# Optimization experiments

Hardware: AMD Instinct MI355X
Metric: run time of the kernel (lower is better)

The kernel has to match this reference:

```python
import jax, jax.numpy as jnp
import numpy as np

ROPE_BASE = 10000.0
NEG_INF = -1e30


def _rope(x, positions):
    """x: [B, heads, D]; positions: [B] int. Matches PrecomputedRotaryEmbedding
    with emb = cat(freqs, freqs) and rotate-half."""
    D = x.shape[-1]
    half = D // 2
    inv_freq = 1.0 / (ROPE_BASE ** (jnp.arange(0, D, 2, dtype=jnp.float32) / D))  # [D/2]
    freqs = positions.astype(jnp.float32)[:, None] * inv_freq[None, :]            # [B, D/2]
    emb = jnp.concatenate([freqs, freqs], axis=-1)                                # [B, D]
    cos = jnp.cos(emb)[:, None, :]
    sin = jnp.sin(emb)[:, None, :]
    x1, x2 = x[..., :half], x[..., half:]
    rotated = jnp.concatenate([-x2, x1], axis=-1)
    return x * cos + rotated * sin


def setup_inputs() -> dict:
    key = jax.random.key(0)
    ks = jax.random.split(key, 6)
    B, H, Hkv, D = 32, 32, 8, 128
    block_size, max_blocks = 16, 256
    num_blocks = B * max_blocks  # 8192, disjoint blocks per sequence
    return {
        "query": jax.random.normal(ks[0], (B, H, D), dtype=jnp.float32),
        "key": jax.random.normal(ks[1], (B, Hkv, D), dtype=jnp.float32),
        "value": jax.random.normal(ks[2], (B, Hkv, D), dtype=jnp.float32),
        "k_cache": jax.random.normal(ks[3], (num_blocks, block_size, Hkv, D), dtype=jnp.float32),
        "v_cache": jax.random.normal(ks[4], (num_blocks, block_size, Hkv, D), dtype=jnp.float32),
        "block_table": jnp.arange(B * max_blocks, dtype=jnp.int32).reshape(B, max_blocks),
        "context_lens": jax.random.randint(ks[5], (B,), 1, 4096, dtype=jnp.int32),
        "block_size": block_size,
    }


def reference(query, key, value, k_cache, v_cache, block_table, context_lens, block_size):
    B, H, D = query.shape
    Hkv = key.shape[1]
    G = H // Hkv
    num_blocks, bs = k_cache.shape[0], k_cache.shape[1]
    scale = D ** -0.5

    # 1) RoPE at position = context_len (as in the original forward)
    q = _rope(query, context_lens)                      # [B, H, D]
    k_new = _rope(key, context_lens)                    # [B, Hkv, D]

    # 2) scatter-store new KV at slot of token (context_len - 1)
    last = context_lens - 1
    slots = block_table[jnp.arange(B), last // block_size] * block_size + last % block_size
    kc = k_cache.reshape(num_blocks * bs, Hkv, D).at[slots].set(k_new)
    vc = v_cache.reshape(num_blocks * bs, Hkv, D).at[slots].set(value)
    kc = kc.reshape(num_blocks, bs, Hkv, D)
    vc = vc.reshape(num_blocks, bs, Hkv, D)

    # 3) gather paged KV per sequence via block_table
    S = block_table.shape[1] * bs                       # max seq len
    Kg = kc[block_table].reshape(B, S, Hkv, D)          # [B, S, Hkv, D]
    Vg = vc[block_table].reshape(B, S, Hkv, D)

    # 4) GQA attention over valid positions [0, context_len)
    qg = q.reshape(B, Hkv, G, D)
    scores = jnp.einsum('bkgd,bskd->bkgs', qg, Kg) * scale   # [B, Hkv, G, S]
    valid = (jnp.arange(S)[None, :] < context_lens[:, None])  # [B, S]
    scores = jnp.where(valid[:, None, None, :], scores, NEG_INF)
    probs = jax.nn.softmax(scores, axis=-1)
    out = jnp.einsum('bkgs,bskd->bkgd', probs, Vg).reshape(B, H, D)
    return out
```

## Files before the change

kernel.cpp:

```cpp
#include <hip/hip_runtime.h>
#include <math.h>

namespace {
constexpr int B   = 32;
constexpr int H   = 32;
constexpr int HKV = 8;
constexpr int D   = 128;
constexpr int G   = H / HKV;
constexpr int BS  = 16;
constexpr int MAXB = 256;
constexpr int S   = BS * MAXB;
constexpr float SCALE = 0.08838834764831845f;
}

struct F8 { float v[8]; };

__device__ __forceinline__ F8 load8(const float* __restrict__ p) {
    F8 r;
    const float4 a = *reinterpret_cast<const float4*>(p);
    const float4 b = *reinterpret_cast<const float4*>(p + 4);
    r.v[0]=a.x; r.v[1]=a.y; r.v[2]=a.z; r.v[3]=a.w;
    r.v[4]=b.x; r.v[5]=b.y; r.v[6]=b.z; r.v[7]=b.w;
    return r;
}

__global__ void rope_kernel(const float* __restrict__ query,
                            const float* __restrict__ key,
                            const int*   __restrict__ ctx,
                            float* __restrict__ q_out,
                            float* __restrict__ k_out)
{
    const int row = blockIdx.x;
    const int t   = threadIdx.x;
    const bool is_q = row < B * H;
    const float* src;
    float* dst;
    int b;
    if (is_q) { b = row / H;  src = query + (size_t)row * D; dst = q_out + (size_t)row * D; }
    else      { int r = row - B * H; b = r / HKV;
                src = key + (size_t)r * D;  dst = k_out + (size_t)r * D; }
    const float pos = (float)ctx[b];
    const float inv = powf(10000.0f, -(2.0f * t) / (float)D);
    const float f = pos * inv;
    const float c = cosf(f), s = sinf(f);
    const float x1 = src[t], x2 = src[t + 64];
    float o1 = x1 * c - x2 * s;
    float o2 = x2 * c + x1 * s;
    if (is_q) { o1 *= SCALE; o2 *= SCALE; }
    dst[t]      = o1;
    dst[t + 64] = o2;
}

__global__ __launch_bounds__(256, 4)
void attn_kernel(const float* __restrict__ qr,
                 const float* __restrict__ kr,
                 const float* __restrict__ vnew,
                 const float* __restrict__ kc,
                 const float* __restrict__ vc,
                 const int*   __restrict__ bt,
                 const int*   __restrict__ ctx,
                 float* __restrict__ pl,
                 float* __restrict__ pa,
                 int chunk, int nch)
{
    const int c  = blockIdx.x;
    const int kv = blockIdx.y;
    const int b  = blockIdx.z;
    const int len = ctx[b];
    const int start = c * chunk;
    if (start >= len) return;
    const int end  = min(start + chunk, len);
    const int lim  = (end == len) ? len - 1 : end;

    const int tid  = threadIdx.x;
    const int lane = tid & 63;
    const int wave = tid >> 6;
    const int sg   = lane >> 4;
    const int t    = lane & 15;
    const int wsub = wave * 4 + sg;

    F8 q[G];
    {
        const float* qbase = qr + ((size_t)b * H + kv * G) * D + t * 8;
        #pragma unroll
        for (int g = 0; g < G; ++g) q[g] = load8(qbase + g * D);
    }

    float l[G];
    F8 acc[G];
    #pragma unroll
    for (int g = 0; g < G; ++g) {
        l[g] = 0.f;
        #pragma unroll
        for (int j = 0; j < 8; ++j) acc[g].v[j] = 0.f;
    }

    const int* btb = bt + b * MAXB + (start >> 4);
    const int e0 = btb[0], e1 = btb[1], e2 = btb[2], e3 = btb[3];

    auto rowaddr = [&](int e) -> size_t {
        return ((size_t)(e * BS + wsub) * HKV + kv) * D + t * 8;
    };
    const size_t a0 = rowaddr(e0), a1 = rowaddr(e1),
                 a2 = rowaddr(e2), a3 = rowaddr(e3);

    auto process = [&](const F8& k, const F8& v) {
        #pragma unroll
        for (int g = 0; g < G; ++g) {
            float s = 0.f;
            #pragma unroll
            for (int j = 0; j < 8; ++j) s += q[g].v[j] * k.v[j];
            s += __shfl_xor(s, 1);
            s += __shfl_xor(s, 2);
            s += __shfl_xor(s, 4);
            s += __shfl_xor(s, 8);
            const float pv = __expf(s);
            l[g] += pv;
            #pragma unroll
            for (int j = 0; j < 8; ++j) acc[g].v[j] += pv * v.v[j];
        }
    };

    const int pw = start + wsub;
    const bool v0 = pw      < lim;
    const bool v1 = pw + 16 < lim;
    const bool v2 = pw + 32 < lim;
    const bool v3 = pw + 48 < lim;

    F8 kk, vv;
    if (v0) { kk = load8(kc + a0); vv = load8(vc + a0); }
    if (v1) { F8 kn = load8(kc + a1), vn = load8(vc + a1);
              process(kk, vv); kk = kn; vv = vn; }
    if (v2) { F8 kn = load8(kc + a2), vn = load8(vc + a2);
              process(kk, vv); kk = kn; vv = vn; }
    if (v3) { F8 kn = load8(kc + a3), vn = load8(vc + a3);
              process(kk, vv); kk = kn; vv = vn; }
    if (v0) process(kk, vv);

    if (end == len && ((len - 1 - start) & 15) == wsub) {
        const size_t off = ((size_t)b * HKV + kv) * D + t * 8;
        F8 k = load8(kr + off), v = load8(vnew + off);
        process(k, v);
    }

    #pragma unroll
    for (int g = 0; g < G; ++g) {
        l[g] += __shfl_xor(l[g], 16);
        l[g] += __shfl_xor(l[g], 32);
        #pragma unroll
        for (int j = 0; j < 8; ++j) {
            acc[g].v[j] += __shfl_xor(acc[g].v[j], 16);
            acc[g].v[j] += __shfl_xor(acc[g].v[j], 32);
        }
    }

    __shared__ float sm_l[4][G];
    __shared__ float sm_acc[4][G][D];
    if (sg == 0) {
        #pragma unroll
        for (int g = 0; g < G; ++g) {
            if (t == 0) sm_l[wave][g] = l[g];
            #pragma unroll
            for (int j = 0; j < 8; ++j) sm_acc[wave][g][t * 8 + j] = acc[g].v[j];
        }
    }
    __syncthreads();

    for (int idx = tid; idx < G * D; idx += 256) {
        const int g = idx >> 7, d = idx & 127;
        const float A = sm_acc[0][g][d] + sm_acc[1][g][d] +
                        sm_acc[2][g][d] + sm_acc[3][g][d];
        const size_t pi = (((size_t)b * HKV + kv) * nch + c) * G + g;
        if (d == 0)
            pl[pi] = sm_l[0][g] + sm_l[1][g] + sm_l[2][g] + sm_l[3][g];
        pa[pi * D + d] = A;
    }
}

__global__ void combine_kernel(const float* __restrict__ pl,
                               const float* __restrict__ pa,
                               const int*   __restrict__ ctx,
                               float* __restrict__ out,
                               int chunk, int nch)
{
    const int bk = blockIdx.x;
    const int b  = bk / HKV;
    const int kv = bk % HKV;
    const int len = ctx[b];
    const int nc = min(nch, (len + chunk - 1) / chunk);
    const int g = threadIdx.x >> 7;
    const int d = threadIdx.x & 127;

    const size_t base = (((size_t)b * HKV + kv) * nch) * G + g;
    float L = 0.f, A = 0.f;
    for (int c = 0; c < nc; ++c) {
        const size_t pi = base + (size_t)c * G;
        L += pl[pi];
        A += pa[pi * D + d];
    }
    out[((size_t)b * H + kv * G + g) * D + d] = A / L;
}

extern "C" void kernel_launch(void* const* d_in, const int* in_sizes, int n_in,
                              void* d_out, int out_size, void* d_ws, size_t ws_size,
                              hipStream_t stream) {
    const float* query   = (const float*)d_in[0];
    const float* key     = (const float*)d_in[1];
    const float* value   = (const float*)d_in[2];
    const float* k_cache = (const float*)d_in[3];
    const float* v_cache = (const float*)d_in[4];
    const int*   bt      = (const int*)d_in[5];
    const int*   ctx     = (const int*)d_in[6];
    float* out = (float*)d_out;
    float* ws  = (float*)d_ws;

    float* qr = ws;
    float* kr = qr + (size_t)B * H * D;
    float* pbase = kr + (size_t)B * HKV * D;
    const size_t fixed_bytes = ((size_t)B * H * D + (size_t)B * HKV * D) * 4;

    int chunk = 64;
    int nch = (S + chunk - 1) / chunk;
    auto need = [&](int n) {
        return fixed_bytes + (size_t)B * HKV * n * G * (1 + D) * 4;
    };
    while (need(nch) > ws_size && chunk < S) {
        chunk *= 2;
        nch = (S + chunk - 1) / chunk;
    }

    float* pl = pbase;
    float* pa = pl + (size_t)B * HKV * nch * G;

    rope_kernel<<<B * (H + HKV), 64, 0, stream>>>(query, key, ctx, qr, kr);

    dim3 grid(nch, HKV, B);
    attn_kernel<<<grid, 256, 0, stream>>>(qr, kr, value, k_cache, v_cache,
                                          bt, ctx, pl, pa, chunk, nch);

    combine_kernel<<<B * HKV, 512, 0, stream>>>(pl, pa, ctx, out, chunk, nch);
}
```

Measured before the change: 151.6 us.

## Use 32-lane row groups with float4 per thread to cut registers

Each KV row is now handled by 32 lanes holding 4 floats each, where before it was 16 lanes holding 8 floats, so the 256-thread block covers 8 rows per step and walks 8 steps per 64-token chunk. This halves the q and acc register footprint, and launch bounds are raised to 8 blocks per SM to raise occupancy for better latency hiding on the memory-bound KV stream. In exchange it adds an extra shuffle stage per score reduction and loads less data per thread in each step.

Measured after the change: 151.5 us. About the same (-0.1%).

```diff
diff --git a/kernel.cpp b/kernel.cpp
--- a/kernel.cpp
+++ b/kernel.cpp
@@ -11,17 +11,6 @@
 constexpr int MAXB = 256;
 constexpr int S   = BS * MAXB;
 constexpr float SCALE = 0.08838834764831845f;
-}
-
-struct F8 { float v[8]; };
-
-__device__ __forceinline__ F8 load8(const float* __restrict__ p) {
-    F8 r;
-    const float4 a = *reinterpret_cast<const float4*>(p);
-    const float4 b = *reinterpret_cast<const float4*>(p + 4);
-    r.v[0]=a.x; r.v[1]=a.y; r.v[2]=a.z; r.v[3]=a.w;
-    r.v[4]=b.x; r.v[5]=b.y; r.v[6]=b.z; r.v[7]=b.w;
-    return r;
 }
 
 __global__ void rope_kernel(const float* __restrict__ query,
@@ -51,7 +40,7 @@
     dst[t + 64] = o2;
 }
 
-__global__ __launch_bounds__(256, 4)
+__global__ __launch_bounds__(256, 8)
 void attn_kernel(const float* __restrict__ qr,
                  const float* __restrict__ kr,
                  const float* __restrict__ vnew,
@@ -69,99 +58,101 @@
     const int len = ctx[b];
     const int start = c * chunk;
     if (start >= len) return;
-    const int end  = min(start + chunk, len);
-    const int lim  = (end == len) ? len - 1 : end;
+    const int end = min(start + chunk, len);
+    const int lim = (end == len) ? len - 1 : end;
 
     const int tid  = threadIdx.x;
-    const int lane = tid & 63;
     const int wave = tid >> 6;
-    const int sg   = lane >> 4;
-    const int t    = lane & 15;
-    const int wsub = wave * 4 + sg;
-
-    F8 q[G];
+    const int half = (tid >> 5) & 1;
+    const int sgp  = tid >> 5;
+    const int t    = tid & 31;
+
+    float4 q[G];
     {
-        const float* qbase = qr + ((size_t)b * H + kv * G) * D + t * 8;
+        const float* qbase = qr + ((size_t)b * H + kv * G) * D + t * 4;
         #pragma unroll
-        for (int g = 0; g < G; ++g) q[g] = load8(qbase + g * D);
+        for (int g = 0; g < G; ++g)
+            q[g] = *reinterpret_cast<const float4*>(qbase + g * D);
     }
 
     float l[G];
-    F8 acc[G];
+    float4 acc[G];
     #pragma unroll
     for (int g = 0; g < G; ++g) {
         l[g] = 0.f;
-        #pragma unroll
-        for (int j = 0; j < 8; ++j) acc[g].v[j] = 0.f;
+        acc[g] = make_float4(0.f, 0.f, 0.f, 0.f);
     }
 
     const int* btb = bt + b * MAXB + (start >> 4);
-    const int e0 = btb[0], e1 = btb[1], e2 = btb[2], e3 = btb[3];
-
-    auto rowaddr = [&](int e) -> size_t {
-        return ((size_t)(e * BS + wsub) * HKV + kv) * D + t * 8;
+    const int e[4] = { btb[0], btb[1], btb[2], btb[3] };
+
+    auto rowbase = [&](int k) -> size_t {
+        const int slot = sgp + 8 * (k & 1);
+        return ((size_t)(e[k >> 1] * BS + slot) * HKV + kv) * D + t * 4;
     };
-    const size_t a0 = rowaddr(e0), a1 = rowaddr(e1),
-                 a2 = rowaddr(e2), a3 = rowaddr(e3);
-
-    auto process = [&](const F8& k, const F8& v) {
+
+    auto process = [&](const float4& k4, const float4& v4) {
         #pragma unroll
         for (int g = 0; g < G; ++g) {
-            float s = 0.f;
-            #pragma unroll
-            for (int j = 0; j < 8; ++j) s += q[g].v[j] * k.v[j];
+            float s = q[g].x * k4.x + q[g].y * k4.y + q[g].z * k4.z + q[g].w * k4.w;
             s += __shfl_xor(s, 1);
             s += __shfl_xor(s, 2);
             s += __shfl_xor(s, 4);
             s += __shfl_xor(s, 8);
+            s += __shfl_xor(s, 16);
             const float pv = __expf(s);
             l[g] += pv;
-            #pragma unroll
-            for (int j = 0; j < 8; ++j) acc[g].v[j] += pv * v.v[j];
+            acc[g].x += pv * v4.x;
+            acc[g].y += pv * v4.y;
+            acc[g].z += pv * v4.z;
+            acc[g].w += pv * v4.w;
         }
     };
 
-    const int pw = start + wsub;
-    const bool v0 = pw      < lim;
-    const bool v1 = pw + 16 < lim;
-    const bool v2 = pw + 32 < lim;
-    const bool v3 = pw + 48 < lim;
-
-    F8 kk, vv;
-    if (v0) { kk = load8(kc + a0); vv = load8(vc + a0); }
-    if (v1) { F8 kn = load8(kc + a1), vn = load8(vc + a1);
-              process(kk, vv); kk = kn; vv = vn; }
-    if (v2) { F8 kn = load8(kc + a2), vn = load8(vc + a2);
-              process(kk, vv); kk = kn; vv = vn; }
-    if (v3) { F8 kn = load8(kc + a3), vn = load8(vc + a3);
-              process(kk, vv); kk = kn; vv = vn; }
-    if (v0) process(kk, vv);
-
-    if (end == len && ((len - 1 - start) & 15) == wsub) {
-        const size_t off = ((size_t)b * HKV + kv) * D + t * 8;
-        F8 k = load8(kr + off), v = load8(vnew + off);
-        process(k, v);
+    const int pw = start + sgp;
+    float4 kk, vv;
+    {
+        const size_t r0 = rowbase(0);
+        if (pw < lim) {
+            kk = *reinterpret_cast<const float4*>(kc + r0);
+            vv = *reinterpret_cast<const float4*>(vc + r0);
+        }
+    }
+    #pragma unroll
+    for (int k = 1; k < 8; ++k) {
+        if (pw + 8 * k < lim) {
+            const size_t rk = rowbase(k);
+            const float4 kn = *reinterpret_cast<const float4*>(kc + rk);
+            const float4 vn = *reinterpret_cast<const float4*>(vc + rk);
+            process(kk, vv);
+            kk = kn; vv = vn;
+        }
+    }
+    if (pw < lim) process(kk, vv);
+
+    if (end == len && ((len - 1 - start) & 7) == sgp) {
+        const size_t off = ((size_t)b * HKV + kv) * D + t * 4;
+        const float4 k4 = *reinterpret_cast<const float4*>(kr + off);
+        const float4 v4 = *reinterpret_cast<const float4*>(vnew + off);
+        process(k4, v4);
     }
 
     #pragma unroll
     for (int g = 0; g < G; ++g) {
-        l[g] += __shfl_xor(l[g], 16);
         l[g] += __shfl_xor(l[g], 32);
-        #pragma unroll
-        for (int j = 0; j < 8; ++j) {
-            acc[g].v[j] += __shfl_xor(acc[g].v[j], 16);
-            acc[g].v[j] += __shfl_xor(acc[g].v[j], 32);
-        }
+        acc[g].x += __shfl_xor(acc[g].x, 32);
+        acc[g].y += __shfl_xor(acc[g].y, 32);
+        acc[g].z += __shfl_xor(acc[g].z, 32);
+        acc[g].w += __shfl_xor(acc[g].w, 32);
     }
 
     __shared__ float sm_l[4][G];
     __shared__ float sm_acc[4][G][D];
-    if (sg == 0) {
+    if (half == 0) {
         #pragma unroll
         for (int g = 0; g < G; ++g) {
             if (t == 0) sm_l[wave][g] = l[g];
-            #pragma unroll
-            for (int j = 0; j < 8; ++j) sm_acc[wave][g][t * 8 + j] = acc[g].v[j];
+            *reinterpret_cast<float4*>(&sm_acc[wave][g][t * 4]) = acc[g];
         }
     }
     __syncthreads();
```
